# Optimization experiments

Hardware: AMD Instinct MI355X
Metric: run time of the kernel (lower is better)

## Reference

```python
import jax, jax.numpy as jnp
import numpy as np

EMBED_DIM = 2048
NUM_HEADS = 16
HEAD_DIM = EMBED_DIM // NUM_HEADS
SCALE = EMBED_DIM ** -0.5  # NOTE: original uses full embed_dim, not head_dim


def setup_inputs() -> dict:
    key = jax.random.key(0)
    ks = jax.random.split(key, 9)
    d = EMBED_DIM
    s = 1.0 / np.sqrt(d)
    inp = {
        "x": jax.random.normal(ks[0], (2, 2048, d), dtype=jnp.float32),
        "wq": jax.random.uniform(ks[1], (d, d), jnp.float32, -s, s),
        "bq": jnp.zeros((d,), jnp.float32),
        "wk": jax.random.uniform(ks[2], (d, d), jnp.float32, -s, s),
        "bk": jnp.zeros((d,), jnp.float32),
        "wv": jax.random.uniform(ks[3], (d, d), jnp.float32, -s, s),
        "bv": jnp.zeros((d,), jnp.float32),
        "wo": jax.random.uniform(ks[4], (d, d), jnp.float32, -s, s),
        "bo": jnp.zeros((d,), jnp.float32),
    }
    return inp


def reference(x, wq, bq, wk, bk, wv, bv, wo, bo):
    b, t, d = x.shape
    h, hd = NUM_HEADS, HEAD_DIM
    # projections (torch Linear: x @ W.T + b; here weights stored as [in, out])
    q = (x @ wq + bq).reshape(b, t, h, hd).transpose(0, 2, 1, 3)  # [b,h,t,hd]
    k = (x @ wk + bk).reshape(b, t, h, hd).transpose(0, 2, 1, 3)
    v = (x @ wv + bv).reshape(b, t, h, hd).transpose(0, 2, 1, 3)
    scores = jnp.einsum("bhqd,bhkd->bhqk", q, k) * SCALE
    probs = jax.nn.softmax(scores, axis=-1)
    attn = jnp.einsum("bhqk,bhkd->bhqd", probs, v)
    attn = attn.transpose(0, 2, 1, 3).reshape(b, t, d)
    return attn @ wo + bo
```

## Files before the change

kernel.cpp:

```cpp
#include <hip/hip_runtime.h>

typedef unsigned int u32;
typedef __bf16 bf16;
typedef bf16 bf16x4 __attribute__((ext_vector_type(4)));
typedef bf16 bf16x8 __attribute__((ext_vector_type(8)));
typedef float f32x4 __attribute__((ext_vector_type(4)));

#define T_ 2048
#define D_ 2048
#define H_ 16
#define HD_ 128
#define SCALE_ 0.022097086912079608f

typedef __attribute__((address_space(1))) u32 gu32;
typedef __attribute__((address_space(3))) u32 lu32;

__device__ __forceinline__ void gload_lds16(const void* g, void* l) {
  __builtin_amdgcn_global_load_lds((gu32*)(void*)g, (lu32*)l, 16, 0, 0);
}

__global__ void cast_x_kernel(const float* __restrict__ x, bf16* __restrict__ xb) {
  int i = blockIdx.x * 256 + threadIdx.x;
  float4 v = ((const float4*)x)[i];
  bf16x4 o;
  o.x = (bf16)v.x; o.y = (bf16)v.y; o.z = (bf16)v.z; o.w = (bf16)v.w;
  ((bf16x4*)xb)[i] = o;
}

__global__ void twcast_kernel(const float* __restrict__ w0, const float* __restrict__ w1,
                              const float* __restrict__ w2, const float* __restrict__ w3,
                              bf16* __restrict__ o0, bf16* __restrict__ o1,
                              bf16* __restrict__ o2, bf16* __restrict__ o3) {
  int z = blockIdx.z;
  const float* W = (z == 0) ? w0 : (z == 1) ? w1 : (z == 2) ? w2 : w3;
  bf16* O = (z == 0) ? o0 : (z == 1) ? o1 : (z == 2) ? o2 : o3;
  __shared__ float tile[64][65];
  int t = threadIdx.x, tx = t & 15, ty = t >> 4;
  int n0 = blockIdx.x * 64, k0 = blockIdx.y * 64;
#pragma unroll
  for (int i = 0; i < 4; i++) {
    float4 v = *(const float4*)&W[(size_t)(k0 + ty + i * 16) * D_ + n0 + tx * 4];
    tile[ty + i * 16][tx * 4 + 0] = v.x;
    tile[ty + i * 16][tx * 4 + 1] = v.y;
    tile[ty + i * 16][tx * 4 + 2] = v.z;
    tile[ty + i * 16][tx * 4 + 3] = v.w;
  }
  __syncthreads();
#pragma unroll
  for (int i = 0; i < 4; i++) {
    int n = ty + i * 16;
    bf16x4 o;
    o.x = (bf16)tile[tx * 4 + 0][n];
    o.y = (bf16)tile[tx * 4 + 1][n];
    o.z = (bf16)tile[tx * 4 + 2][n];
    o.w = (bf16)tile[tx * 4 + 3][n];
    *(bf16x4*)&O[(size_t)(n0 + n) * D_ + k0 + tx * 4] = o;
  }
}

__device__ __forceinline__ void gemm_core_128(const bf16* __restrict__ A,
                                              const bf16* __restrict__ Bt,
                                              f32x4 acc[4][4], int m0, int n0) {
  __shared__ char smem[32768];
  char* aT = smem;
  char* bT = smem + 16384;
  const int t = threadIdx.x;
  const int lane = t & 63;
  const int wr = (t >> 7) & 1;
  const int wc = (t >> 6) & 1;
  for (int k0 = 0; k0 < 2048; k0 += 64) {
    __syncthreads();
#pragma unroll
    for (int i = 0; i < 4; i++) {
      int L = i * 4096 + t * 16;
      int row = L >> 7;
      int kb = (L & 127) ^ ((row & 7) << 4);
      gload_lds16(A + (size_t)(m0 + row) * 2048 + k0 + (kb >> 1), aT + L);
      gload_lds16(Bt + (size_t)(n0 + row) * 2048 + k0 + (kb >> 1), bT + L);
    }
    __syncthreads();
#pragma unroll
    for (int kk = 0; kk < 2; kk++) {
      int ak = kk * 64 + ((lane >> 4) << 4);
      bf16x8 af[4], bfv[4];
#pragma unroll
      for (int f = 0; f < 4; f++) {
        int ar = wr * 64 + f * 16 + (lane & 15);
        af[f] = *(const bf16x8*)(aT + ar * 128 + (ak ^ ((ar & 7) << 4)));
        int br = wc * 64 + f * 16 + (lane & 15);
        bfv[f] = *(const bf16x8*)(bT + br * 128 + (ak ^ ((br & 7) << 4)));
      }
#pragma unroll
      for (int mi = 0; mi < 4; mi++)
#pragma unroll
        for (int ni = 0; ni < 4; ni++)
          acc[mi][ni] = __builtin_amdgcn_mfma_f32_16x16x32_bf16(af[mi], bfv[ni], acc[mi][ni], 0, 0, 0);
    }
  }
}

__global__ __launch_bounds__(256, 2) void qkv_gemm_kernel(
    const bf16* __restrict__ xb,
    const bf16* __restrict__ wqt, const bf16* __restrict__ wkt, const bf16* __restrict__ wvt,
    const float* __restrict__ bq, const float* __restrict__ bk, const float* __restrict__ bv,
    bf16* __restrict__ Qb, bf16* __restrict__ Kb, bf16* __restrict__ Vb) {
  const bf16* Bt; const float* bias; bf16* Out; float scale;
  int z = blockIdx.z;
  if (z == 0)      { Bt = wqt; bias = bq; Out = Qb; scale = SCALE_; }
  else if (z == 1) { Bt = wkt; bias = bk; Out = Kb; scale = 1.0f; }
  else             { Bt = wvt; bias = bv; Out = Vb; scale = 1.0f; }
  int m0 = blockIdx.y * 128, n0 = blockIdx.x * 128;
  f32x4 zero = {0.f, 0.f, 0.f, 0.f};
  f32x4 acc[4][4];
#pragma unroll
  for (int mi = 0; mi < 4; mi++)
#pragma unroll
    for (int ni = 0; ni < 4; ni++) acc[mi][ni] = zero;
  gemm_core_128(xb, Bt, acc, m0, n0);
  int lane = threadIdx.x & 63;
  int wr = (threadIdx.x >> 7) & 1, wc = (threadIdx.x >> 6) & 1;
#pragma unroll
  for (int ni = 0; ni < 4; ni++) {
    int cn = n0 + wc * 64 + ni * 16 + (lane & 15);
    float bb = bias[cn];
    int h = cn >> 7, hd = cn & 127;
#pragma unroll
    for (int mi = 0; mi < 4; mi++) {
      int rm = m0 + wr * 64 + mi * 16 + ((lane >> 4) << 2);
#pragma unroll
      for (int r = 0; r < 4; r++) {
        int mg = rm + r;
        int b = mg >> 11, tt = mg & 2047;
        Out[(size_t)((b * H_ + h) * T_ + tt) * HD_ + hd] = (bf16)((acc[mi][ni][r] + bb) * scale);
      }
    }
  }
}

__global__ void vtr_kernel(const bf16* __restrict__ V, bf16* __restrict__ Vt) {
  __shared__ bf16 tile[64][72];
  int t = threadIdx.x, tx = t & 15, ty = t >> 4;
  int t0 = blockIdx.x * 64, hd0 = blockIdx.y * 64, bh = blockIdx.z;
  const bf16* Vi = V + (size_t)bh * T_ * HD_;
  bf16* Vo = Vt + (size_t)bh * HD_ * T_;
#pragma unroll
  for (int i = 0; i < 4; i++) {
    bf16x4 v = *(const bf16x4*)&Vi[(size_t)(t0 + ty + i * 16) * HD_ + hd0 + tx * 4];
    tile[ty + i * 16][tx * 4 + 0] = v.x;
    tile[ty + i * 16][tx * 4 + 1] = v.y;
    tile[ty + i * 16][tx * 4 + 2] = v.z;
    tile[ty + i * 16][tx * 4 + 3] = v.w;
  }
  __syncthreads();
#pragma unroll
  for (int i = 0; i < 4; i++) {
    int hd = ty + i * 16;
    bf16x4 v;
    v.x = tile[tx * 4 + 0][hd];
    v.y = tile[tx * 4 + 1][hd];
    v.z = tile[tx * 4 + 2][hd];
    v.w = tile[tx * 4 + 3][hd];
    *(bf16x4*)&Vo[(size_t)(hd0 + hd) * T_ + t0 + tx * 4] = v;
  }
}

__global__ __launch_bounds__(256, 2) void attn_kernel(
    const bf16* __restrict__ Qb, const bf16* __restrict__ Kb,
    const bf16* __restrict__ Vtb, bf16* __restrict__ Ab) {
  __shared__ char smem[49152];
  char* Klds = smem;
  char* Vlds = smem + 16384;
  char* Plds = smem + 32768;
  const int t = threadIdx.x, lane = t & 63, w = t >> 6;
  const int bh = blockIdx.y;
  const int q0 = blockIdx.x * 128;
  const bf16* Qh = Qb + (size_t)bh * T_ * HD_;
  const bf16* Kh = Kb + (size_t)bh * T_ * HD_;
  const bf16* Vh = Vtb + (size_t)bh * HD_ * T_;

  bf16x8 qf[2][4];
#pragma unroll
  for (int mi = 0; mi < 2; mi++)
#pragma unroll
    for (int kf = 0; kf < 4; kf++) {
      int row = q0 + w * 32 + mi * 16 + (lane & 15);
      int hd = kf * 32 + ((lane >> 4) << 3);
      qf[mi][kf] = *(const bf16x8*)(Qh + (size_t)row * HD_ + hd);
    }

  f32x4 zero = {0.f, 0.f, 0.f, 0.f};
  f32x4 o[2][8];
#pragma unroll
  for (int mi = 0; mi < 2; mi++)
#pragma unroll
    for (int nf = 0; nf < 8; nf++) o[mi][nf] = zero;
  float mrow[2][4], lrow[2][4];
#pragma unroll
  for (int mi = 0; mi < 2; mi++)
#pragma unroll
    for (int r = 0; r < 4; r++) { mrow[mi][r] = -1e30f; lrow[mi][r] = 0.f; }

  for (int kt = 0; kt < T_; kt += 64) {
#pragma unroll
    for (int i = 0; i < 4; i++) {
      int L = i * 4096 + t * 16;
      int rowK = L >> 8;
      int kbK = (L & 255) ^ ((rowK & 7) << 4);
      gload_lds16(Kh + (size_t)(kt + rowK) * HD_ + (kbK >> 1), Klds + L);
      int rowV = L >> 7;
      int kbV = (L & 127) ^ ((rowV & 7) << 4);
      gload_lds16(Vh + (size_t)rowV * T_ + kt + (kbV >> 1), Vlds + L);
    }
    __syncthreads();

    f32x4 s[2][4];
#pragma unroll
    for (int mi = 0; mi < 2; mi++)
#pragma unroll
      for (int nf = 0; nf < 4; nf++) s[mi][nf] = zero;
#pragma unroll
    for (int kf = 0; kf < 4; kf++) {
      int kb = kf * 64 + ((lane >> 4) << 4);
      bf16x8 kfr[4];
#pragma unroll
      for (int nf = 0; nf < 4; nf++) {
        int rr = nf * 16 + (lane & 15);
        kfr[nf] = *(const bf16x8*)(Klds + rr * 256 + (kb ^ ((rr & 7) << 4)));
      }
#pragma unroll
      for (int mi = 0; mi < 2; mi++)
#pragma unroll
        for (int nf = 0; nf < 4; nf++)
          s[mi][nf] = __builtin_amdgcn_mfma_f32_16x16x32_bf16(qf[mi][kf], kfr[nf], s[mi][nf], 0, 0, 0);
    }

#pragma unroll
    for (int mi = 0; mi < 2; mi++) {
#pragma unroll
      for (int r = 0; r < 4; r++) {
        float mx = fmaxf(fmaxf(s[mi][0][r], s[mi][1][r]), fmaxf(s[mi][2][r], s[mi][3][r]));
        mx = fmaxf(mx, __shfl_xor(mx, 1));
        mx = fmaxf(mx, __shfl_xor(mx, 2));
        mx = fmaxf(mx, __shfl_xor(mx, 4));
        mx = fmaxf(mx, __shfl_xor(mx, 8));
        float mnew = fmaxf(mrow[mi][r], mx);
        float fac = __expf(mrow[mi][r] - mnew);
        mrow[mi][r] = mnew;
        float rs = 0.f;
#pragma unroll
        for (int nf = 0; nf < 4; nf++) {
          float p = __expf(s[mi][nf][r] - mnew);
          s[mi][nf][r] = p;
          rs += p;
        }
        rs += __shfl_xor(rs, 1);
        rs += __shfl_xor(rs, 2);
        rs += __shfl_xor(rs, 4);
        rs += __shfl_xor(rs, 8);
        lrow[mi][r] = lrow[mi][r] * fac + rs;
#pragma unroll
        for (int nf = 0; nf < 8; nf++) o[mi][nf][r] *= fac;
        int row = w * 32 + mi * 16 + ((lane >> 4) << 2) + r;
#pragma unroll
        for (int nf = 0; nf < 4; nf++) {
          int cb = (nf * 32 + (lane & 15) * 2) ^ ((row & 7) << 4);
          *(bf16*)(Plds + row * 128 + cb) = (bf16)s[mi][nf][r];
        }
      }
    }

#pragma unroll
    for (int kf = 0; kf < 2; kf++) {
      int kb = kf * 64 + ((lane >> 4) << 4);
      bf16x8 pf[2];
#pragma unroll
      for (int mi = 0; mi < 2; mi++) {
        int rr = w * 32 + mi * 16 + (lane & 15);
        pf[mi] = *(const bf16x8*)(Plds + rr * 128 + (kb ^ ((rr & 7) << 4)));
      }
#pragma unroll
      for (int nf = 0; nf < 8; nf++) {
        int rr = nf * 16 + (lane & 15);
        bf16x8 vf = *(const bf16x8*)(Vlds + rr * 128 + (kb ^ ((rr & 7) << 4)));
#pragma unroll
        for (int mi = 0; mi < 2; mi++)
          o[mi][nf] = __builtin_amdgcn_mfma_f32_16x16x32_bf16(pf[mi], vf, o[mi][nf], 0, 0, 0);
      }
    }
    __syncthreads();
  }

  int b = bh >> 4, h = bh & 15;
#pragma unroll
  for (int mi = 0; mi < 2; mi++)
#pragma unroll
    for (int r = 0; r < 4; r++) {
      float inv = 1.f / lrow[mi][r];
      int tq = q0 + w * 32 + mi * 16 + ((lane >> 4) << 2) + r;
      size_t base = ((size_t)b * T_ + tq) * D_ + h * HD_;
#pragma unroll
      for (int nf = 0; nf < 8; nf++) {
        int hd = nf * 16 + (lane & 15);
        Ab[base + hd] = (bf16)(o[mi][nf][r] * inv);
      }
    }
}

__global__ __launch_bounds__(256, 2) void out_gemm_kernel(
    const bf16* __restrict__ Ab, const bf16* __restrict__ wot,
    const float* __restrict__ bo, float* __restrict__ out) {
  int m0 = blockIdx.y * 128, n0 = blockIdx.x * 128;
  f32x4 zero = {0.f, 0.f, 0.f, 0.f};
  f32x4 acc[4][4];
#pragma unroll
  for (int mi = 0; mi < 4; mi++)
#pragma unroll
    for (int ni = 0; ni < 4; ni++) acc[mi][ni] = zero;
  gemm_core_128(Ab, wot, acc, m0, n0);
  int lane = threadIdx.x & 63;
  int wr = (threadIdx.x >> 7) & 1, wc = (threadIdx.x >> 6) & 1;
#pragma unroll
  for (int ni = 0; ni < 4; ni++) {
    int cn = n0 + wc * 64 + ni * 16 + (lane & 15);
    float bb = bo[cn];
#pragma unroll
    for (int mi = 0; mi < 4; mi++) {
      int rm = m0 + wr * 64 + mi * 16 + ((lane >> 4) << 2);
#pragma unroll
      for (int r = 0; r < 4; r++)
        out[(size_t)(rm + r) * D_ + cn] = acc[mi][ni][r] + bb;
    }
  }
}

extern "C" void kernel_launch(void* const* d_in, const int* in_sizes, int n_in,
                              void* d_out, int out_size, void* d_ws, size_t ws_size,
                              hipStream_t stream) {
  const float* x  = (const float*)d_in[0];
  const float* wq = (const float*)d_in[1];
  const float* bq = (const float*)d_in[2];
  const float* wk = (const float*)d_in[3];
  const float* bk = (const float*)d_in[4];
  const float* wv = (const float*)d_in[5];
  const float* bv = (const float*)d_in[6];
  const float* wo = (const float*)d_in[7];
  const float* bo = (const float*)d_in[8];
  float* out = (float*)d_out;
  char* ws = (char*)d_ws;

  bf16* xb  = (bf16*)(ws);
  bf16* wqt = (bf16*)(ws + 16777216);
  bf16* wkt = (bf16*)(ws + 25165824);
  bf16* wvt = (bf16*)(ws + 33554432);
  bf16* wot = (bf16*)(ws + 41943040);
  bf16* Qb  = (bf16*)(ws + 50331648);
  bf16* Kb  = (bf16*)(ws + 67108864);
  bf16* Vb  = (bf16*)(ws + 83886080);
  bf16* Vtb = (bf16*)(ws + 100663296);
  bf16* Ab  = xb;

  cast_x_kernel<<<8192, 256, 0, stream>>>(x, xb);
  twcast_kernel<<<dim3(32, 32, 4), 256, 0, stream>>>(wq, wk, wv, wo, wqt, wkt, wvt, wot);
  qkv_gemm_kernel<<<dim3(16, 32, 3), 256, 0, stream>>>(xb, wqt, wkt, wvt, bq, bk, bv, Qb, Kb, Vb);
  vtr_kernel<<<dim3(32, 2, 32), 256, 0, stream>>>(Vb, Vtb);
  attn_kernel<<<dim3(16, 32), 256, 0, stream>>>(Qb, Kb, Vtb, Ab);
  out_gemm_kernel<<<dim3(16, 32), 256, 0, stream>>>(Ab, wot, bo, out);

  (void)in_sizes; (void)n_in; (void)out_size; (void)ws_size;
}
```

Measured before the change: 435.0 us.

## Double-buffer GEMM LDS tiles and shrink attention query tile with exp2 lazy rescale

The shared GEMM core now double-buffers its A/B LDS tiles, so the global-to-LDS load of the next k-slice overlaps MFMA work on the current one, with one barrier per step. The attention kernel halves its query tile to 64 rows (one 16-row fragment per wave), doubles the grid and raises the occupancy hint to 4 blocks per CU. The log2(e) factor is folded into the Q scale so softmax can use exp2f. The running max is updated only when a new max exceeds the old one by more than 8, which skips most rescales of the output accumulators. The trade-offs are twice the GEMM LDS footprint, which may cap occupancy, K/V tiles loaded twice as often per query, and lazy-max numerics that can let unnormalised probabilities grow up to 2^8.

```diff
diff --git a/kernel.cpp b/kernel.cpp
--- a/kernel.cpp
+++ b/kernel.cpp
@@ -11,6 +11,7 @@
 #define H_ 16
 #define HD_ 128
 #define SCALE_ 0.022097086912079608f
+#define LOG2E_ 1.4426950408889634f
 
 typedef __attribute__((address_space(1))) u32 gu32;
 typedef __attribute__((address_space(3))) u32 lu32;
@@ -58,45 +59,62 @@
   }
 }
 
+__device__ __forceinline__ void stage_tile(const bf16* __restrict__ A,
+                                           const bf16* __restrict__ Bt,
+                                           char* aT, char* bT,
+                                           int m0, int n0, int k0, int t) {
+#pragma unroll
+  for (int i = 0; i < 4; i++) {
+    int L = i * 4096 + t * 16;
+    int row = L >> 7;
+    int kb = (L & 127) ^ ((row & 7) << 4);
+    gload_lds16(A + (size_t)(m0 + row) * 2048 + k0 + (kb >> 1), aT + L);
+    gload_lds16(Bt + (size_t)(n0 + row) * 2048 + k0 + (kb >> 1), bT + L);
+  }
+}
+
+__device__ __forceinline__ void gemm_compute64(const char* aT, const char* bT,
+                                               f32x4 acc[4][4], int lane, int wr, int wc) {
+#pragma unroll
+  for (int kk = 0; kk < 2; kk++) {
+    int ak = kk * 64 + ((lane >> 4) << 4);
+    bf16x8 af[4], bfv[4];
+#pragma unroll
+    for (int f = 0; f < 4; f++) {
+      int ar = wr * 64 + f * 16 + (lane & 15);
+      af[f] = *(const bf16x8*)(aT + ar * 128 + (ak ^ ((ar & 7) << 4)));
+      int br = wc * 64 + f * 16 + (lane & 15);
+      bfv[f] = *(const bf16x8*)(bT + br * 128 + (ak ^ ((br & 7) << 4)));
+    }
+#pragma unroll
+    for (int mi = 0; mi < 4; mi++)
+#pragma unroll
+      for (int ni = 0; ni < 4; ni++)
+        acc[mi][ni] = __builtin_amdgcn_mfma_f32_16x16x32_bf16(af[mi], bfv[ni], acc[mi][ni], 0, 0, 0);
+  }
+}
+
 __device__ __forceinline__ void gemm_core_128(const bf16* __restrict__ A,
                                               const bf16* __restrict__ Bt,
                                               f32x4 acc[4][4], int m0, int n0) {
-  __shared__ char smem[32768];
-  char* aT = smem;
-  char* bT = smem + 16384;
+  __shared__ char smem[65536];
   const int t = threadIdx.x;
   const int lane = t & 63;
   const int wr = (t >> 7) & 1;
   const int wc = (t >> 6) & 1;
-  for (int k0 = 0; k0 < 2048; k0 += 64) {
+  stage_tile(A, Bt, smem, smem + 16384, m0, n0, 0, t);
+  __syncthreads();
+  int cur = 0;
+  for (int k0 = 64; k0 < 2048; k0 += 64) {
+    char* base = smem + (cur ^ 1) * 32768;
+    stage_tile(A, Bt, base, base + 16384, m0, n0, k0, t);
+    char* cbase = smem + cur * 32768;
+    gemm_compute64(cbase, cbase + 16384, acc, lane, wr, wc);
     __syncthreads();
-#pragma unroll
-    for (int i = 0; i < 4; i++) {
-      int L = i * 4096 + t * 16;
-      int row = L >> 7;
-      int kb = (L & 127) ^ ((row & 7) << 4);
-      gload_lds16(A + (size_t)(m0 + row) * 2048 + k0 + (kb >> 1), aT + L);
-      gload_lds16(Bt + (size_t)(n0 + row) * 2048 + k0 + (kb >> 1), bT + L);
-    }
-    __syncthreads();
-#pragma unroll
-    for (int kk = 0; kk < 2; kk++) {
-      int ak = kk * 64 + ((lane >> 4) << 4);
-      bf16x8 af[4], bfv[4];
-#pragma unroll
-      for (int f = 0; f < 4; f++) {
-        int ar = wr * 64 + f * 16 + (lane & 15);
-        af[f] = *(const bf16x8*)(aT + ar * 128 + (ak ^ ((ar & 7) << 4)));
-        int br = wc * 64 + f * 16 + (lane & 15);
-        bfv[f] = *(const bf16x8*)(bT + br * 128 + (ak ^ ((br & 7) << 4)));
-      }
-#pragma unroll
-      for (int mi = 0; mi < 4; mi++)
-#pragma unroll
-        for (int ni = 0; ni < 4; ni++)
-          acc[mi][ni] = __builtin_amdgcn_mfma_f32_16x16x32_bf16(af[mi], bfv[ni], acc[mi][ni], 0, 0, 0);
-    }
-  }
+    cur ^= 1;
+  }
+  char* cbase = smem + cur * 32768;
+  gemm_compute64(cbase, cbase + 16384, acc, lane, wr, wc);
 }
 
 __global__ __launch_bounds__(256, 2) void qkv_gemm_kernel(
@@ -106,7 +124,7 @@
     bf16* __restrict__ Qb, bf16* __restrict__ Kb, bf16* __restrict__ Vb) {
   const bf16* Bt; const float* bias; bf16* Out; float scale;
   int z = blockIdx.z;
-  if (z == 0)      { Bt = wqt; bias = bq; Out = Qb; scale = SCALE_; }
+  if (z == 0)      { Bt = wqt; bias = bq; Out = Qb; scale = SCALE_ * LOG2E_; }
   else if (z == 1) { Bt = wkt; bias = bk; Out = Kb; scale = 1.0f; }
   else             { Bt = wvt; bias = bv; Out = Vb; scale = 1.0f; }
   int m0 = blockIdx.y * 128, n0 = blockIdx.x * 128;
@@ -164,41 +182,35 @@
   }
 }
 
-__global__ __launch_bounds__(256, 2) void attn_kernel(
+__global__ __launch_bounds__(256, 4) void attn_kernel(
     const bf16* __restrict__ Qb, const bf16* __restrict__ Kb,
     const bf16* __restrict__ Vtb, bf16* __restrict__ Ab) {
-  __shared__ char smem[49152];
+  __shared__ char smem[40960];
   char* Klds = smem;
   char* Vlds = smem + 16384;
   char* Plds = smem + 32768;
   const int t = threadIdx.x, lane = t & 63, w = t >> 6;
   const int bh = blockIdx.y;
-  const int q0 = blockIdx.x * 128;
+  const int q0 = blockIdx.x * 64;
   const bf16* Qh = Qb + (size_t)bh * T_ * HD_;
   const bf16* Kh = Kb + (size_t)bh * T_ * HD_;
   const bf16* Vh = Vtb + (size_t)bh * HD_ * T_;
 
-  bf16x8 qf[2][4];
-#pragma unroll
-  for (int mi = 0; mi < 2; mi++)
-#pragma unroll
-    for (int kf = 0; kf < 4; kf++) {
-      int row = q0 + w * 32 + mi * 16 + (lane & 15);
-      int hd = kf * 32 + ((lane >> 4) << 3);
-      qf[mi][kf] = *(const bf16x8*)(Qh + (size_t)row * HD_ + hd);
-    }
+  bf16x8 qf[4];
+#pragma unroll
+  for (int kf = 0; kf < 4; kf++) {
+    int row = q0 + w * 16 + (lane & 15);
+    int hd = kf * 32 + ((lane >> 4) << 3);
+    qf[kf] = *(const bf16x8*)(Qh + (size_t)row * HD_ + hd);
+  }
 
   f32x4 zero = {0.f, 0.f, 0.f, 0.f};
-  f32x4 o[2][8];
-#pragma unroll
-  for (int mi = 0; mi < 2; mi++)
-#pragma unroll
-    for (int nf = 0; nf < 8; nf++) o[mi][nf] = zero;
-  float mrow[2][4], lrow[2][4];
-#pragma unroll
-  for (int mi = 0; mi < 2; mi++)
-#pragma unroll
-    for (int r = 0; r < 4; r++) { mrow[mi][r] = -1e30f; lrow[mi][r] = 0.f; }
+  f32x4 o[8];
+#pragma unroll
+  for (int nf = 0; nf < 8; nf++) o[nf] = zero;
+  float mrow[4], lrow[4];
+#pragma unroll
+  for (int r = 0; r < 4; r++) { mrow[r] = -1e30f; lrow[r] = 0.f; }
 
   for (int kt = 0; kt < T_; kt += 64) {
 #pragma unroll
@@ -213,11 +225,9 @@
     }
     __syncthreads();
 
-    f32x4 s[2][4];
-#pragma unroll
-    for (int mi = 0; mi < 2; mi++)
-#pragma unroll
-      for (int nf = 0; nf < 4; nf++) s[mi][nf] = zero;
+    f32x4 s[4];
+#pragma unroll
+    for (int nf = 0; nf < 4; nf++) s[nf] = zero;
 #pragma unroll
     for (int kf = 0; kf < 4; kf++) {
       int kb = kf * 64 + ((lane >> 4) << 4);
@@ -228,63 +238,55 @@
         kfr[nf] = *(const bf16x8*)(Klds + rr * 256 + (kb ^ ((rr & 7) << 4)));
       }
 #pragma unroll
-      for (int mi = 0; mi < 2; mi++)
-#pragma unroll
-        for (int nf = 0; nf < 4; nf++)
-          s[mi][nf] = __builtin_amdgcn_mfma_f32_16x16x32_bf16(qf[mi][kf], kfr[nf], s[mi][nf], 0, 0, 0);
-    }
-
-#pragma unroll
-    for (int mi = 0; mi < 2; mi++) {
-#pragma unroll
-      for (int r = 0; r < 4; r++) {
-        float mx = fmaxf(fmaxf(s[mi][0][r], s[mi][1][r]), fmaxf(s[mi][2][r], s[mi][3][r]));
-        mx = fmaxf(mx, __shfl_xor(mx, 1));
-        mx = fmaxf(mx, __shfl_xor(mx, 2));
-        mx = fmaxf(mx, __shfl_xor(mx, 4));
-        mx = fmaxf(mx, __shfl_xor(mx, 8));
-        float mnew = fmaxf(mrow[mi][r], mx);
-        float fac = __expf(mrow[mi][r] - mnew);
-        mrow[mi][r] = mnew;
-        float rs = 0.f;
-#pragma unroll
-        for (int nf = 0; nf < 4; nf++) {
-          float p = __expf(s[mi][nf][r] - mnew);
-          s[mi][nf][r] = p;
-          rs += p;
-        }
-        rs += __shfl_xor(rs, 1);
-        rs += __shfl_xor(rs, 2);
-        rs += __shfl_xor(rs, 4);
-        rs += __shfl_xor(rs, 8);
-        lrow[mi][r] = lrow[mi][r] * fac + rs;
-#pragma unroll
-        for (int nf = 0; nf < 8; nf++) o[mi][nf][r] *= fac;
-        int row = w * 32 + mi * 16 + ((lane >> 4) << 2) + r;
-#pragma unroll
-        for (int nf = 0; nf < 4; nf++) {
-          int cb = (nf * 32 + (lane & 15) * 2) ^ ((row & 7) << 4);
-          *(bf16*)(Plds + row * 128 + cb) = (bf16)s[mi][nf][r];
-        }
+      for (int nf = 0; nf < 4; nf++)
+        s[nf] = __builtin_amdgcn_mfma_f32_16x16x32_bf16(qf[kf], kfr[nf], s[nf], 0, 0, 0);
+    }
+
+#pragma unroll
+    for (int r = 0; r < 4; r++) {
+      float mx = fmaxf(fmaxf(s[0][r], s[1][r]), fmaxf(s[2][r], s[3][r]));
+      mx = fmaxf(mx, __shfl_xor(mx, 1));
+      mx = fmaxf(mx, __shfl_xor(mx, 2));
+      mx = fmaxf(mx, __shfl_xor(mx, 4));
+      mx = fmaxf(mx, __shfl_xor(mx, 8));
+      if (mx > mrow[r] + 8.f) {
+        float fac = exp2f(mrow[r] - mx);
+        mrow[r] = mx;
+        lrow[r] *= fac;
+#pragma unroll
+        for (int nf = 0; nf < 8; nf++) o[nf][r] *= fac;
+      }
+      float m = mrow[r];
+      float rs = 0.f;
+#pragma unroll
+      for (int nf = 0; nf < 4; nf++) {
+        float p = exp2f(s[nf][r] - m);
+        s[nf][r] = p;
+        rs += p;
+      }
+      rs += __shfl_xor(rs, 1);
+      rs += __shfl_xor(rs, 2);
+      rs += __shfl_xor(rs, 4);
+      rs += __shfl_xor(rs, 8);
+      lrow[r] += rs;
+      int row = w * 16 + ((lane >> 4) << 2) + r;
+#pragma unroll
+      for (int nf = 0; nf < 4; nf++) {
+        int cb = (nf * 32 + (lane & 15) * 2) ^ ((row & 7) << 4);
+        *(bf16*)(Plds + row * 128 + cb) = (bf16)s[nf][r];
       }
     }
 
 #pragma unroll
     for (int kf = 0; kf < 2; kf++) {
       int kb = kf * 64 + ((lane >> 4) << 4);
-      bf16x8 pf[2];
-#pragma unroll
-      for (int mi = 0; mi < 2; mi++) {
-        int rr = w * 32 + mi * 16 + (lane & 15);
-        pf[mi] = *(const bf16x8*)(Plds + rr * 128 + (kb ^ ((rr & 7) << 4)));
-      }
+      int rr = w * 16 + (lane & 15);
+      bf16x8 pf = *(const bf16x8*)(Plds + rr * 128 + (kb ^ ((rr & 7) << 4)));
 #pragma unroll
       for (int nf = 0; nf < 8; nf++) {
-        int rr = nf * 16 + (lane & 15);
-        bf16x8 vf = *(const bf16x8*)(Vlds + rr * 128 + (kb ^ ((rr & 7) << 4)));
-#pragma unroll
-        for (int mi = 0; mi < 2; mi++)
-          o[mi][nf] = __builtin_amdgcn_mfma_f32_16x16x32_bf16(pf[mi], vf, o[mi][nf], 0, 0, 0);
+        int vr = nf * 16 + (lane & 15);
+        bf16x8 vf = *(const bf16x8*)(Vlds + vr * 128 + (kb ^ ((vr & 7) << 4)));
+        o[nf] = __builtin_amdgcn_mfma_f32_16x16x32_bf16(pf, vf, o[nf], 0, 0, 0);
       }
     }
     __syncthreads();
@@ -292,18 +294,16 @@
 
   int b = bh >> 4, h = bh & 15;
 #pragma unroll
-  for (int mi = 0; mi < 2; mi++)
-#pragma unroll
-    for (int r = 0; r < 4; r++) {
-      float inv = 1.f / lrow[mi][r];
-      int tq = q0 + w * 32 + mi * 16 + ((lane >> 4) << 2) + r;
-      size_t base = ((size_t)b * T_ + tq) * D_ + h * HD_;
-#pragma unroll
-      for (int nf = 0; nf < 8; nf++) {
-        int hd = nf * 16 + (lane & 15);
-        Ab[base + hd] = (bf16)(o[mi][nf][r] * inv);
-      }
-    }
+  for (int r = 0; r < 4; r++) {
+    float inv = 1.f / lrow[r];
+    int tq = q0 + w * 16 + ((lane >> 4) << 2) + r;
+    size_t base = ((size_t)b * T_ + tq) * D_ + h * HD_;
+#pragma unroll
+    for (int nf = 0; nf < 8; nf++) {
+      int hd = nf * 16 + (lane & 15);
+      Ab[base + hd] = (bf16)(o[nf][r] * inv);
+    }
+  }
 }
 
 __global__ __launch_bounds__(256, 2) void out_gemm_kernel(
@@ -363,7 +363,7 @@
   twcast_kernel<<<dim3(32, 32, 4), 256, 0, stream>>>(wq, wk, wv, wo, wqt, wkt, wvt, wot);
   qkv_gemm_kernel<<<dim3(16, 32, 3), 256, 0, stream>>>(xb, wqt, wkt, wvt, bq, bk, bv, Qb, Kb, Vb);
   vtr_kernel<<<dim3(32, 2, 32), 256, 0, stream>>>(Vb, Vtb);
-  attn_kernel<<<dim3(16, 32), 256, 0, stream>>>(Qb, Kb, Vtb, Ab);
+  attn_kernel<<<dim3(32, 32), 256, 0, stream>>>(Qb, Kb, Vtb, Ab);
   out_gemm_kernel<<<dim3(16, 32), 256, 0, stream>>>(Ab, wot, bo, out);
 
   (void)in_sizes; (void)n_in; (void)out_size; (void)ws_size;
```

After: 462.6 us. 1.06x slower.
